# Optimization experiments

Hardware: AMD Instinct MI355X
Metric: run time of the kernel (lower is better)

## Reference

```python
import jax, jax.numpy as jnp
import numpy as np

B, T, C = 2, 2048, 1024
H = 16
HD = C // H  # 64


def setup_inputs() -> dict:
    key = jax.random.key(0)
    k1, k2, k3, k4, k5 = jax.random.split(key, 5)
    s = 0.02
    return {
        "x": jax.random.normal(k1, (B, T, C), dtype=jnp.float32),
        "w_attn": jax.random.normal(k2, (C, 3 * C), dtype=jnp.float32) * s,
        "b_attn": jnp.zeros((3 * C,), dtype=jnp.float32),
        "w_proj": jax.random.normal(k3, (C, C), dtype=jnp.float32) * s,
        "b_proj": jnp.zeros((C,), dtype=jnp.float32),
    }


def reference(x, w_attn, b_attn, w_proj, b_proj):
    Bx, Tx, Cx = x.shape
    qkv = x @ w_attn + b_attn                      # [B,T,3C]
    q, k, v = jnp.split(qkv, 3, axis=-1)
    # [B,T,C] -> [B,H,T,HD]
    def heads(t):
        return t.reshape(Bx, Tx, H, HD).transpose(0, 2, 1, 3)
    q, k, v = heads(q), heads(k), heads(v)
    scale = 1.0 / np.sqrt(HD).astype(np.float32)
    scores = jnp.einsum("bhqd,bhkd->bhqk", q, k) * scale
    causal = jnp.tril(jnp.ones((Tx, Tx), dtype=bool))
    scores = jnp.where(causal, scores, -jnp.inf)
    attn = jax.nn.softmax(scores, axis=-1)          # dropout p=0 -> identity
    y = jnp.einsum("bhqk,bhkd->bhqd", attn, v)
    y = y.transpose(0, 2, 1, 3).reshape(Bx, Tx, Cx)
    return y @ w_proj + b_proj
```

## Files before the change

kernel.cpp:

```cpp
#include <hip/hip_runtime.h>
#include <hip/hip_bf16.h>

#define Bb 2
#define Tt 2048
#define Cc 1024
#define Hh 16
#define HD 64
#define QS 0.18033688f

typedef __attribute__((ext_vector_type(8))) short bf16x8;
typedef __attribute__((ext_vector_type(4))) short bf16x4;
typedef __attribute__((ext_vector_type(4))) float f32x4;
typedef __attribute__((ext_vector_type(2))) unsigned int u32x2;

__device__ inline short f2b(float f) {
    unsigned int u = __builtin_bit_cast(unsigned int, f);
    unsigned int r = (u + 0x7FFFu + ((u >> 16) & 1u)) >> 16;
    return (short)(unsigned short)r;
}

__device__ inline void gl16(const void* g, void* l) {
    __builtin_amdgcn_global_load_lds(
        (const __attribute__((address_space(1))) void*)g,
        (__attribute__((address_space(3))) void*)l, 16, 0, 0);
}

__global__ __launch_bounds__(256) void prep_kernel(
    const float* __restrict__ x, short* __restrict__ xbf,
    const float* __restrict__ wA, short* __restrict__ wAT,
    const float* __restrict__ wP, short* __restrict__ wPT)
{
    const int bx = blockIdx.x, tid = threadIdx.x;
    if (bx < 2048) {
        int i = (bx * 256 + tid) * 8;
        float4 a = *(const float4*)(x + i);
        float4 b = *(const float4*)(x + i + 4);
        bf16x8 v;
        v[0] = f2b(a.x); v[1] = f2b(a.y); v[2] = f2b(a.z); v[3] = f2b(a.w);
        v[4] = f2b(b.x); v[5] = f2b(b.y); v[6] = f2b(b.z); v[7] = f2b(b.w);
        *(bf16x8*)(xbf + i) = v;
        return;
    }
    const float* W; short* WT; int N, t;
    if (bx < 2816) { t = bx - 2048; W = wA; WT = wAT; N = 3072; }
    else           { t = bx - 2816; W = wP; WT = wPT; N = 1024; }
    const int K = 1024;
    int k0 = (t & 15) * 64, n0 = (t >> 4) * 64;
    int nl = tid & 63, kg = tid >> 6;
    int n = n0 + nl;
    short v[16];
#pragma unroll
    for (int i = 0; i < 16; i++)
        v[i] = f2b(W[(size_t)(k0 + kg * 16 + i) * N + n]);
    short* dst = WT + (size_t)n * K + k0 + kg * 16;
    *(bf16x8*)dst = *(bf16x8*)&v[0];
    *(bf16x8*)(dst + 8) = *(bf16x8*)&v[8];
}

__global__ __launch_bounds__(256) void gemm_qkv(
    const short* __restrict__ A, const short* __restrict__ Bt,
    const float* __restrict__ bias,
    short* __restrict__ qw, short* __restrict__ kw, short* __restrict__ vTw,
    int M, int N, int K)
{
    __shared__ __attribute__((aligned(16))) short SH[17408];

    const int tid  = threadIdx.x;
    const int wave = tid >> 6, lane = tid & 63;
    const int quad = lane >> 4, lr = lane & 15;
    const int wm = wave >> 1, wn = wave & 1;
    const int m0 = blockIdx.y * 128, n0 = blockIdx.x * 128;

    int srow[2], scol[2];
#pragma unroll
    for (int i = 0; i < 2; i++) {
        int id = i * 256 + tid;
        srow[i] = id >> 2;
        scol[i] = ((id & 3) ^ ((srow[i] >> 1) & 3)) << 3;
    }
    const int pfrag = quad ^ ((lr >> 1) & 3);

    f32x4 acc[4][4];
    const f32x4 zf = {0.f, 0.f, 0.f, 0.f};
#pragma unroll
    for (int mi = 0; mi < 4; mi++)
#pragma unroll
        for (int ni = 0; ni < 4; ni++) acc[mi][ni] = zf;

#pragma unroll
    for (int i = 0; i < 2; i++) {
        gl16(A + (size_t)(m0 + srow[i]) * K + scol[i], &SH[(i * 256 + tid) * 8]);
        gl16(Bt + (size_t)(n0 + srow[i]) * K + scol[i], &SH[8192 + (i * 256 + tid) * 8]);
    }

    const int iters = K >> 5;
    for (int it = 0; it < iters; ++it) {
        const int co = (it & 1) * 4096;
        const int no = ((it & 1) ^ 1) * 4096;
        __syncthreads();
        if (it + 1 < iters) {
            const int k1 = (it + 1) << 5;
#pragma unroll
            for (int i = 0; i < 2; i++) {
                gl16(A + (size_t)(m0 + srow[i]) * K + k1 + scol[i],
                     &SH[no + (i * 256 + tid) * 8]);
                gl16(Bt + (size_t)(n0 + srow[i]) * K + k1 + scol[i],
                     &SH[8192 + no + (i * 256 + tid) * 8]);
            }
        }
        bf16x8 af[4], bf[4];
#pragma unroll
        for (int mi = 0; mi < 4; mi++) {
            int row = wm * 64 + mi * 16 + lr;
            af[mi] = *(bf16x8*)&SH[co + (row * 4 + pfrag) * 8];
        }
#pragma unroll
        for (int ni = 0; ni < 4; ni++) {
            int row = wn * 64 + ni * 16 + lr;
            bf[ni] = *(bf16x8*)&SH[8192 + co + (row * 4 + pfrag) * 8];
        }
#pragma unroll
        for (int mi = 0; mi < 4; mi++)
#pragma unroll
            for (int ni = 0; ni < 4; ni++)
                acc[mi][ni] = __builtin_amdgcn_mfma_f32_16x16x32_bf16(
                    af[mi], bf[ni], acc[mi][ni], 0, 0, 0);
    }

    if (n0 < 2048) {
#pragma unroll
        for (int mi = 0; mi < 4; mi++) {
#pragma unroll
            for (int ni = 0; ni < 4; ni++) {
                int c = n0 + wn * 64 + ni * 16 + lr;
                float bv = bias[c];
#pragma unroll
                for (int r = 0; r < 4; r++) {
                    int rg = m0 + wm * 64 + mi * 16 + quad * 4 + r;
                    float val = acc[mi][ni][r] + bv;
                    int which = c >> 10, cc = c & 1023;
                    int h = cc >> 6, d = cc & 63;
                    int b = rg >> 11, t = rg & 2047;
                    size_t bh = (size_t)b * Hh + h;
                    if (which == 0) qw[(bh * Tt + t) * HD + d] = f2b(val * QS);
                    else            kw[(bh * Tt + t) * HD + d] = f2b(val);
                }
            }
        }
    } else {
        __syncthreads();
#pragma unroll
        for (int ni = 0; ni < 4; ni++) {
            int cl = wn * 64 + ni * 16 + lr;
            float bv = bias[n0 + cl];
#pragma unroll
            for (int mi = 0; mi < 4; mi++)
#pragma unroll
                for (int r = 0; r < 4; r++) {
                    int tl = wm * 64 + mi * 16 + quad * 4 + r;
                    SH[cl * 136 + tl] = f2b(acc[mi][ni][r] + bv);
                }
        }
        __syncthreads();
        const int rl = tid >> 1, half = tid & 1;
        const int cc = (n0 & 1023) + rl;
        const int h = cc >> 6, d = cc & 63;
        const int b = m0 >> 11, tb = (m0 & 2047) + half * 64;
        short* dst = vTw + (((size_t)b * Hh + h) * HD + d) * Tt + tb;
        const short* src = &SH[rl * 136 + half * 64];
#pragma unroll
        for (int jj = 0; jj < 8; jj++)
            *(bf16x8*)(dst + jj * 8) = *(const bf16x8*)(src + jj * 8);
    }
}

__global__ __launch_bounds__(256) void gemm_proj(
    const short* __restrict__ A, const short* __restrict__ Bt,
    const float* __restrict__ bias, float* __restrict__ out,
    int M, int N, int K)
{
    __shared__ __attribute__((aligned(16))) short SH[12288];

    const int tid  = threadIdx.x;
    const int wave = tid >> 6, lane = tid & 63;
    const int quad = lane >> 4, lr = lane & 15;
    const int wm = wave >> 1, wn = wave & 1;
    const int m0 = blockIdx.y * 64, n0 = blockIdx.x * 128;

    const int arow = tid >> 2;
    const int acol = ((tid & 3) ^ ((arow >> 1) & 3)) << 3;
    int brow[2], bcol[2];
#pragma unroll
    for (int i = 0; i < 2; i++) {
        int id = i * 256 + tid;
        brow[i] = id >> 2;
        bcol[i] = ((id & 3) ^ ((brow[i] >> 1) & 3)) << 3;
    }
    const int pfrag = quad ^ ((lr >> 1) & 3);

    f32x4 acc[2][4];
    const f32x4 zf = {0.f, 0.f, 0.f, 0.f};
#pragma unroll
    for (int mi = 0; mi < 2; mi++)
#pragma unroll
        for (int ni = 0; ni < 4; ni++) acc[mi][ni] = zf;

    auto asrc = [&](int row, int col) -> const short* {
        int rg = m0 + row, b = rg >> 11, t = rg & 2047;
        int h = col >> 6, d = col & 63;
        return A + ((((size_t)b * Hh + h) * Tt + t) * HD + d);
    };

    gl16(asrc(arow, acol), &SH[tid * 8]);
#pragma unroll
    for (int i = 0; i < 2; i++)
        gl16(Bt + (size_t)(n0 + brow[i]) * K + bcol[i],
             &SH[4096 + (i * 256 + tid) * 8]);

    const int iters = K >> 5;
    for (int it = 0; it < iters; ++it) {
        const int coA = (it & 1) * 2048, noA = ((it & 1) ^ 1) * 2048;
        const int coB = (it & 1) * 4096, noB = ((it & 1) ^ 1) * 4096;
        __syncthreads();
        if (it + 1 < iters) {
            const int k1 = (it + 1) << 5;
            gl16(asrc(arow, k1 + acol), &SH[noA + tid * 8]);
#pragma unroll
            for (int i = 0; i < 2; i++)
                gl16(Bt + (size_t)(n0 + brow[i]) * K + k1 + bcol[i],
                     &SH[4096 + noB + (i * 256 + tid) * 8]);
        }
        bf16x8 af[2], bf[4];
#pragma unroll
        for (int mi = 0; mi < 2; mi++) {
            int row = wm * 32 + mi * 16 + lr;
            af[mi] = *(bf16x8*)&SH[coA + (row * 4 + pfrag) * 8];
        }
#pragma unroll
        for (int ni = 0; ni < 4; ni++) {
            int row = wn * 64 + ni * 16 + lr;
            bf[ni] = *(bf16x8*)&SH[4096 + coB + (row * 4 + pfrag) * 8];
        }
#pragma unroll
        for (int mi = 0; mi < 2; mi++)
#pragma unroll
            for (int ni = 0; ni < 4; ni++)
                acc[mi][ni] = __builtin_amdgcn_mfma_f32_16x16x32_bf16(
                    af[mi], bf[ni], acc[mi][ni], 0, 0, 0);
    }

#pragma unroll
    for (int mi = 0; mi < 2; mi++)
#pragma unroll
        for (int ni = 0; ni < 4; ni++) {
            int c = n0 + wn * 64 + ni * 16 + lr;
            float bv = bias[c];
#pragma unroll
            for (int r = 0; r < 4; r++) {
                int rg = m0 + wm * 32 + mi * 16 + quad * 4 + r;
                out[(size_t)rg * N + c] = acc[mi][ni][r] + bv;
            }
        }
}

__global__ __launch_bounds__(256) void gemm_f32src(
    const void* __restrict__ Araw, const float* __restrict__ Bm,
    const float* __restrict__ bias, float* __restrict__ out,
    short* __restrict__ qw, short* __restrict__ kw, short* __restrict__ vTw,
    int M, int N, int K, int mode)
{
    __shared__ __attribute__((aligned(16))) short As[128 * 32];
    __shared__ __attribute__((aligned(16))) short Bs[128 * 32];

    const int tid  = threadIdx.x;
    const int wave = tid >> 6, lane = tid & 63;
    const int quad = lane >> 4, lr = lane & 15;
    const int wm = wave >> 1, wn = wave & 1;
    const int m0 = blockIdx.y * 128, n0 = blockIdx.x * 128;

    f32x4 acc[4][4];
    const f32x4 zf = {0.f, 0.f, 0.f, 0.f};
#pragma unroll
    for (int mi = 0; mi < 4; mi++)
#pragma unroll
        for (int ni = 0; ni < 4; ni++) acc[mi][ni] = zf;

    for (int k0 = 0; k0 < K; k0 += 32) {
        __syncthreads();
        if (mode == 1) {
            const float* Af = (const float*)Araw;
#pragma unroll
            for (int i = 0; i < 4; i++) {
                int id  = i * 256 + tid;
                int row = id >> 3;
                int kc  = (id & 7) << 2;
                float4 v = *(const float4*)(Af + (size_t)(m0 + row) * K + k0 + kc);
                short* d = &As[row * 32 + kc];
                d[0] = f2b(v.x); d[1] = f2b(v.y); d[2] = f2b(v.z); d[3] = f2b(v.w);
            }
        } else {
            const short* Ah = (const short*)Araw;
#pragma unroll
            for (int i = 0; i < 2; i++) {
                int id  = i * 256 + tid;
                int row = id >> 2;
                int kc  = (id & 3) << 3;
                int rg = m0 + row, b = rg >> 11, t = rg & 2047;
                int c = k0 + kc, h = c >> 6, d = c & 63;
                *(bf16x8*)&As[row * 32 + kc] =
                    *(const bf16x8*)(Ah + ((((size_t)b * Hh + h) * Tt + t) * HD + d));
            }
        }
#pragma unroll
        for (int i = 0; i < 4; i++) {
            int id = i * 256 + tid;
            int kr = id >> 5;
            int nc = (id & 31) << 2;
            float4 v = *(const float4*)(Bm + (size_t)(k0 + kr) * N + n0 + nc);
            Bs[(nc + 0) * 32 + kr] = f2b(v.x);
            Bs[(nc + 1) * 32 + kr] = f2b(v.y);
            Bs[(nc + 2) * 32 + kr] = f2b(v.z);
            Bs[(nc + 3) * 32 + kr] = f2b(v.w);
        }
        __syncthreads();

        bf16x8 af[4], bf[4];
#pragma unroll
        for (int mi = 0; mi < 4; mi++)
            af[mi] = *(bf16x8*)&As[(wm * 64 + mi * 16 + lr) * 32 + quad * 8];
#pragma unroll
        for (int ni = 0; ni < 4; ni++)
            bf[ni] = *(bf16x8*)&Bs[(wn * 64 + ni * 16 + lr) * 32 + quad * 8];
#pragma unroll
        for (int mi = 0; mi < 4; mi++)
#pragma unroll
            for (int ni = 0; ni < 4; ni++)
                acc[mi][ni] = __builtin_amdgcn_mfma_f32_16x16x32_bf16(
                    af[mi], bf[ni], acc[mi][ni], 0, 0, 0);
    }

#pragma unroll
    for (int mi = 0; mi < 4; mi++) {
#pragma unroll
        for (int ni = 0; ni < 4; ni++) {
            int c = n0 + wn * 64 + ni * 16 + lr;
            float bv = bias[c];
#pragma unroll
            for (int r = 0; r < 4; r++) {
                int rg = m0 + wm * 64 + mi * 16 + quad * 4 + r;
                float val = acc[mi][ni][r] + bv;
                if (mode == 1) {
                    int which = c >> 10, cc = c & 1023;
                    int h = cc >> 6, d = cc & 63;
                    int b = rg >> 11, t = rg & 2047;
                    size_t bh = (size_t)b * Hh + h;
                    if (which == 0)      qw[(bh * Tt + t) * HD + d] = f2b(val * QS);
                    else if (which == 1) kw[(bh * Tt + t) * HD + d] = f2b(val);
                    else                 vTw[(bh * HD + d) * Tt + t] = f2b(val);
                } else {
                    out[(size_t)rg * N + c] = val;
                }
            }
        }
    }
}

__global__ __launch_bounds__(128) void attn_kernel(
    short* __restrict__ qw, const short* __restrict__ kw,
    const short* __restrict__ vTw)
{
    __shared__ __attribute__((aligned(16))) short Ks[2][4096];
    __shared__ __attribute__((aligned(16))) short Vs[2][4096];

    const int bh = blockIdx.x & 31;
    const int p  = blockIdx.x >> 5;
    const int pB = 63 - p;
    const int tid = threadIdx.x;
    const int wave = tid >> 6, lane = tid & 63;
    const int quad = lane >> 4, lr = lane & 15;

    short* qp = qw + (size_t)bh * Tt * HD;
    const short* kp = kw + (size_t)bh * Tt * HD;
    const short* vp = vTw + (size_t)bh * HD * Tt;

    const int r0m[2] = { p * 32 + wave * 16, pB * 32 + wave * 16 };

    int srow[4], scol[4];
#pragma unroll
    for (int i = 0; i < 4; i++) {
        int id = i * 128 + tid;
        srow[i] = id >> 3;
        scol[i] = ((id & 7) ^ (srow[i] & 7)) << 3;
    }

    bf16x8 aq[2][2];
#pragma unroll
    for (int mt = 0; mt < 2; mt++)
#pragma unroll
        for (int h = 0; h < 2; h++)
            aq[mt][h] = *(const bf16x8*)(qp + (size_t)(r0m[mt] + lr) * HD
                                            + h * 32 + quad * 8);

    const f32x4 zf = {0.f, 0.f, 0.f, 0.f};
    f32x4 o[2][4];
    float lacc[2] = {0.f, 0.f};
#pragma unroll
    for (int mt = 0; mt < 2; mt++)
#pragma unroll
        for (int nt = 0; nt < 4; nt++) o[mt][nt] = zf;

#pragma unroll
    for (int i = 0; i < 4; i++) {
        gl16(kp + (size_t)srow[i] * HD + scol[i], &Ks[0][(i * 128 + tid) * 8]);
        gl16(vp + (size_t)srow[i] * Tt + scol[i], &Vs[0][(i * 128 + tid) * 8]);
    }

    const int clast = (pB * 32 + 31) >> 6;
    for (int c = 0; c <= clast; ++c) {
        const int j0 = c << 6;
        const int cur = c & 1;
        __syncthreads();
        if (c < clast) {
#pragma unroll
            for (int i = 0; i < 4; i++) {
                gl16(kp + (size_t)(j0 + 64 + srow[i]) * HD + scol[i],
                     &Ks[cur ^ 1][(i * 128 + tid) * 8]);
                gl16(vp + (size_t)srow[i] * Tt + (j0 + 64) + scol[i],
                     &Vs[cur ^ 1][(i * 128 + tid) * 8]);
            }
        }
        const short* Kc = &Ks[cur][0];
        const short* Vc = &Vs[cur][0];
#pragma unroll
        for (int kt = 0; kt < 4; kt++) {
            const int k16 = j0 + kt * 16;
            const bool act0 = k16 <= r0m[0] + 15;
            const bool act1 = k16 <= r0m[1] + 15;
            if (!act1 && !act0) break;
            int krow = (kt * 16 + lr) * 8;
            bf16x8 kb0 = *(const bf16x8*)&Kc[(krow + (quad ^ (lr & 7))) * 8];
            bf16x8 kb1 = *(const bf16x8*)&Kc[(krow + ((4 + quad) ^ (lr & 7))) * 8];
            bf16x4 va[4];
#pragma unroll
            for (int nt = 0; nt < 4; nt++) {
                int vrow = (nt * 16 + lr) * 8;
                int slot = (kt * 2 + (quad >> 1)) ^ (lr & 7);
                va[nt] = *(const bf16x4*)&Vc[(vrow + slot) * 8 + (quad & 1) * 4];
            }
#pragma unroll
            for (int mt = 0; mt < 2; mt++) {
                if (!(mt ? act1 : act0)) continue;
                f32x4 s = __builtin_amdgcn_mfma_f32_16x16x32_bf16(
                    kb0, aq[mt][0], zf, 0, 0, 0);
                s = __builtin_amdgcn_mfma_f32_16x16x32_bf16(
                    kb1, aq[mt][1], s, 0, 0, 0);
                const bool needmask = (k16 + 15) > r0m[mt];
                unsigned u[4];
#pragma unroll
                for (int r = 0; r < 4; r++) {
                    float e = __builtin_amdgcn_exp2f(s[r]);
                    if (needmask && (k16 + quad * 4 + r) > (r0m[mt] + lr)) e = 0.f;
                    u[r] = __builtin_bit_cast(unsigned, e);
                    lacc[mt] += __builtin_bit_cast(float, u[r] & 0xFFFF0000u);
                }
                u32x2 pu = { __builtin_amdgcn_perm(u[1], u[0], 0x07060302u),
                             __builtin_amdgcn_perm(u[3], u[2], 0x07060302u) };
                bf16x4 pt = __builtin_bit_cast(bf16x4, pu);
#pragma unroll
                for (int nt = 0; nt < 4; nt++)
                    o[mt][nt] = __builtin_amdgcn_mfma_f32_16x16x16bf16_1k(
                        va[nt], pt, o[mt][nt], 0, 0, 0);
            }
        }
    }

#pragma unroll
    for (int mt = 0; mt < 2; mt++) {
        lacc[mt] += __shfl_xor(lacc[mt], 16, 64);
        lacc[mt] += __shfl_xor(lacc[mt], 32, 64);
        lacc[mt] = 1.0f / lacc[mt];
    }

#pragma unroll
    for (int mt = 0; mt < 2; mt++)
#pragma unroll
        for (int nt = 0; nt < 4; nt++) {
            bf16x4 ov;
#pragma unroll
            for (int r = 0; r < 4; r++) ov[r] = f2b(o[mt][nt][r] * lacc[mt]);
            *(bf16x4*)(qp + (size_t)(r0m[mt] + lr) * HD + nt * 16 + quad * 4) = ov;
        }
}

extern "C" void kernel_launch(void* const* d_in, const int* in_sizes, int n_in,
                              void* d_out, int out_size, void* d_ws, size_t ws_size,
                              hipStream_t stream) {
    const float* x      = (const float*)d_in[0];
    const float* w_attn = (const float*)d_in[1];
    const float* b_attn = (const float*)d_in[2];
    const float* w_proj = (const float*)d_in[3];
    const float* b_proj = (const float*)d_in[4];
    float* out = (float*)d_out;

    const size_t per = (size_t)Bb * Hh * Tt * HD;
    short* qw  = (short*)d_ws;
    short* kw  = qw + per;
    short* vTw = kw + per;
    const int M = Bb * Tt;

    const size_t need_fast = (3 * per + per + (size_t)3072 * 1024 + (size_t)1024 * 1024) * 2;

    if (ws_size >= need_fast) {
        short* xbf = vTw + per;
        short* wAT = xbf + per;
        short* wPT = wAT + (size_t)3072 * 1024;

        prep_kernel<<<dim3(3072), 256, 0, stream>>>(x, xbf, w_attn, wAT, w_proj, wPT);

        gemm_qkv<<<dim3(3 * Cc / 128, M / 128), 256, 0, stream>>>(
            xbf, wAT, b_attn, qw, kw, vTw, M, 3 * Cc, Cc);

        attn_kernel<<<dim3(1024), 128, 0, stream>>>(qw, kw, vTw);

        gemm_proj<<<dim3(Cc / 128, M / 64), 256, 0, stream>>>(
            qw, wPT, b_proj, out, M, Cc, Cc);
    } else {
        gemm_f32src<<<dim3(3 * Cc / 128, M / 128), 256, 0, stream>>>(
            x, w_attn, b_attn, nullptr, qw, kw, vTw, M, 3 * Cc, Cc, 1);

        attn_kernel<<<dim3(1024), 128, 0, stream>>>(qw, kw, vTw);

        gemm_f32src<<<dim3(Cc / 128, M / 128), 256, 0, stream>>>(
            qw, w_proj, b_proj, out, nullptr, nullptr, nullptr, M, Cc, Cc, 2);
    }
}
```

Before: 195.0 us.

## Merge two attention query-pair blocks per workgroup to share K/V tiles

```diff
diff --git a/kernel.cpp b/kernel.cpp
--- a/kernel.cpp
+++ b/kernel.cpp
@@ -365,7 +365,7 @@
     }
 }
 
-__global__ __launch_bounds__(128) void attn_kernel(
+__global__ __launch_bounds__(256) void attn_kernel(
     short* __restrict__ qw, const short* __restrict__ kw,
     const short* __restrict__ vTw)
 {
@@ -373,24 +373,40 @@
     __shared__ __attribute__((aligned(16))) short Vs[2][4096];
 
     const int bh = blockIdx.x & 31;
-    const int p  = blockIdx.x >> 5;
-    const int pB = 63 - p;
+    const int g  = blockIdx.x >> 5;
     const int tid = threadIdx.x;
     const int wave = tid >> 6, lane = tid & 63;
     const int quad = lane >> 4, lr = lane & 15;
 
+    const int pA = 2 * g + (wave >> 1);
+    const int pB = 63 - pA;
+    const int wh = (wave & 1) * 16;
+    const int r0m[2] = { pA * 32 + wh, pB * 32 + wh };
+
     short* qp = qw + (size_t)bh * Tt * HD;
     const short* kp = kw + (size_t)bh * Tt * HD;
     const short* vp = vTw + (size_t)bh * HD * Tt;
 
-    const int r0m[2] = { p * 32 + wave * 16, pB * 32 + wave * 16 };
-
-    int srow[4], scol[4];
-#pragma unroll
-    for (int i = 0; i < 4; i++) {
-        int id = i * 128 + tid;
+    int srow[2], scol[2];
+#pragma unroll
+    for (int i = 0; i < 2; i++) {
+        int id = i * 256 + tid;
         srow[i] = id >> 3;
         scol[i] = ((id & 7) ^ (srow[i] & 7)) << 3;
+    }
+
+    int kbo0[4], kbo1[4], vao[4][4];
+#pragma unroll
+    for (int kt = 0; kt < 4; kt++) {
+        int krow = (kt * 16 + lr) * 8;
+        kbo0[kt] = (krow + (quad ^ (lr & 7))) * 8;
+        kbo1[kt] = (krow + ((4 + quad) ^ (lr & 7))) * 8;
+#pragma unroll
+        for (int nt = 0; nt < 4; nt++) {
+            int vrow = (nt * 16 + lr) * 8;
+            int slot = (kt * 2 + (quad >> 1)) ^ (lr & 7);
+            vao[kt][nt] = (vrow + slot) * 8 + (quad & 1) * 4;
+        }
     }
 
     bf16x8 aq[2][2];
@@ -410,23 +426,23 @@
         for (int nt = 0; nt < 4; nt++) o[mt][nt] = zf;
 
 #pragma unroll
-    for (int i = 0; i < 4; i++) {
-        gl16(kp + (size_t)srow[i] * HD + scol[i], &Ks[0][(i * 128 + tid) * 8]);
-        gl16(vp + (size_t)srow[i] * Tt + scol[i], &Vs[0][(i * 128 + tid) * 8]);
-    }
-
-    const int clast = (pB * 32 + 31) >> 6;
+    for (int i = 0; i < 2; i++) {
+        gl16(kp + (size_t)srow[i] * HD + scol[i], &Ks[0][(i * 256 + tid) * 8]);
+        gl16(vp + (size_t)srow[i] * Tt + scol[i], &Vs[0][(i * 256 + tid) * 8]);
+    }
+
+    const int clast = ((63 - 2 * g) * 32 + 31) >> 6;
     for (int c = 0; c <= clast; ++c) {
         const int j0 = c << 6;
         const int cur = c & 1;
         __syncthreads();
         if (c < clast) {
 #pragma unroll
-            for (int i = 0; i < 4; i++) {
+            for (int i = 0; i < 2; i++) {
                 gl16(kp + (size_t)(j0 + 64 + srow[i]) * HD + scol[i],
-                     &Ks[cur ^ 1][(i * 128 + tid) * 8]);
+                     &Ks[cur ^ 1][(i * 256 + tid) * 8]);
                 gl16(vp + (size_t)srow[i] * Tt + (j0 + 64) + scol[i],
-                     &Vs[cur ^ 1][(i * 128 + tid) * 8]);
+                     &Vs[cur ^ 1][(i * 256 + tid) * 8]);
             }
         }
         const short* Kc = &Ks[cur][0];
@@ -437,16 +453,12 @@
             const bool act0 = k16 <= r0m[0] + 15;
             const bool act1 = k16 <= r0m[1] + 15;
             if (!act1 && !act0) break;
-            int krow = (kt * 16 + lr) * 8;
-            bf16x8 kb0 = *(const bf16x8*)&Kc[(krow + (quad ^ (lr & 7))) * 8];
-            bf16x8 kb1 = *(const bf16x8*)&Kc[(krow + ((4 + quad) ^ (lr & 7))) * 8];
+            bf16x8 kb0 = *(const bf16x8*)&Kc[kbo0[kt]];
+            bf16x8 kb1 = *(const bf16x8*)&Kc[kbo1[kt]];
             bf16x4 va[4];
 #pragma unroll
-            for (int nt = 0; nt < 4; nt++) {
-                int vrow = (nt * 16 + lr) * 8;
-                int slot = (kt * 2 + (quad >> 1)) ^ (lr & 7);
-                va[nt] = *(const bf16x4*)&Vc[(vrow + slot) * 8 + (quad & 1) * 4];
-            }
+            for (int nt = 0; nt < 4; nt++)
+                va[nt] = *(const bf16x4*)&Vc[vao[kt][nt]];
 #pragma unroll
             for (int mt = 0; mt < 2; mt++) {
                 if (!(mt ? act1 : act0)) continue;
@@ -454,14 +466,22 @@
                     kb0, aq[mt][0], zf, 0, 0, 0);
                 s = __builtin_amdgcn_mfma_f32_16x16x32_bf16(
                     kb1, aq[mt][1], s, 0, 0, 0);
-                const bool needmask = (k16 + 15) > r0m[mt];
                 unsigned u[4];
-#pragma unroll
-                for (int r = 0; r < 4; r++) {
-                    float e = __builtin_amdgcn_exp2f(s[r]);
-                    if (needmask && (k16 + quad * 4 + r) > (r0m[mt] + lr)) e = 0.f;
-                    u[r] = __builtin_bit_cast(unsigned, e);
-                    lacc[mt] += __builtin_bit_cast(float, u[r] & 0xFFFF0000u);
+                if (k16 + 15 <= r0m[mt]) {
+#pragma unroll
+                    for (int r = 0; r < 4; r++) {
+                        float e = __builtin_amdgcn_exp2f(s[r]);
+                        u[r] = __builtin_bit_cast(unsigned, e);
+                        lacc[mt] += e;
+                    }
+                } else {
+#pragma unroll
+                    for (int r = 0; r < 4; r++) {
+                        float e = __builtin_amdgcn_exp2f(s[r]);
+                        if ((k16 + quad * 4 + r) > (r0m[mt] + lr)) e = 0.f;
+                        u[r] = __builtin_bit_cast(unsigned, e);
+                        lacc[mt] += e;
+                    }
                 }
                 u32x2 pu = { __builtin_amdgcn_perm(u[1], u[0], 0x07060302u),
                              __builtin_amdgcn_perm(u[3], u[2], 0x07060302u) };
@@ -520,7 +540,7 @@
         gemm_qkv<<<dim3(3 * Cc / 128, M / 128), 256, 0, stream>>>(
             xbf, wAT, b_attn, qw, kw, vTw, M, 3 * Cc, Cc);
 
-        attn_kernel<<<dim3(1024), 128, 0, stream>>>(qw, kw, vTw);
+        attn_kernel<<<dim3(512), 256, 0, stream>>>(qw, kw, vTw);
 
         gemm_proj<<<dim3(Cc / 128, M / 64), 256, 0, stream>>>(
             qw, wPT, b_proj, out, M, Cc, Cc);
@@ -528,7 +548,7 @@
         gemm_f32src<<<dim3(3 * Cc / 128, M / 128), 256, 0, stream>>>(
             x, w_attn, b_attn, nullptr, qw, kw, vTw, M, 3 * Cc, Cc, 1);
 
-        attn_kernel<<<dim3(1024), 128, 0, stream>>>(qw, kw, vTw);
+        attn_kernel<<<dim3(512), 256, 0, stream>>>(qw, kw, vTw);
 
         gemm_f32src<<<dim3(Cc / 128, M / 128), 256, 0, stream>>>(
             qw, w_proj, b_proj, out, nullptr, nullptr, nullptr, M, Cc, Cc, 2);
```

New measurement: 188.6 us. -3.3%, faster.
